# Kernel tuning notes

Hardware: AMD Instinct MI355X
Metric: run time of the kernel (lower is better)

Reference implementation:

```python
import jax, jax.numpy as jnp
import numpy as np

B, S, D, H = 2, 2048, 1024, 16
DK = D // H

def setup_inputs() -> dict:
    key = jax.random.key(0)
    ks = jax.random.split(key, 9)
    s = 1.0 / np.sqrt(D)
    return {
        "query": jax.random.normal(ks[0], (B, S, D), dtype=jnp.float32),
        "Wq": jax.random.uniform(ks[1], (D, D), jnp.float32, -s, s),
        "bq": jax.random.uniform(ks[2], (D,), jnp.float32, -s, s),
        "Wk": jax.random.uniform(ks[3], (D, D), jnp.float32, -s, s),
        "bk": jax.random.uniform(ks[4], (D,), jnp.float32, -s, s),
        "Wv": jax.random.uniform(ks[5], (D, D), jnp.float32, -s, s),
        "bv": jax.random.uniform(ks[6], (D,), jnp.float32, -s, s),
        "Wo": jax.random.uniform(ks[7], (D, D), jnp.float32, -s, s),
        "bo": jax.random.uniform(ks[8], (D,), jnp.float32, -s, s),
    }

def reference(query, Wq, bq, Wk, bk, Wv, bv, Wo, bo):
    # q/k/v projections, reshape to [B,H,S,DK]
    def proj(x, W, b):
        return (x @ W + b).reshape(B, S, H, DK).transpose(0, 2, 1, 3)
    q = proj(query, Wq, bq)
    k = proj(query, Wk, bk)
    v = proj(query, Wv, bv)
    scores = jnp.einsum("bhqd,bhkd->bhqk", q, k) / jnp.sqrt(jnp.float32(DK))
    attn = jax.nn.softmax(scores, axis=-1)
    out = jnp.einsum("bhqk,bhkd->bhqd", attn, v)  # [B,H,S,DK]
    concat = out.transpose(0, 2, 1, 3).reshape(B, S, D)
    return concat @ Wo + bo
```

## Files before the change

kernel.cpp:

```cpp
#include <hip/hip_runtime.h>

#define S_LEN  2048
#define DMODEL 1024
#define NHEAD  16
#define DKDIM  64
#define NBATCH 2

typedef short bf16x8 __attribute__((ext_vector_type(8)));
typedef float f32x4  __attribute__((ext_vector_type(4)));

__device__ __forceinline__ unsigned short f2b(float f){
  unsigned int x = __float_as_uint(f);
  return (unsigned short)((x + 0x7FFFu + ((x >> 16) & 1u)) >> 16);
}
__device__ __forceinline__ unsigned short f2b_rhu(float f){
  return (unsigned short)((__float_as_uint(f) + 0x8000u) >> 16);
}
__device__ __forceinline__ bf16x8 ld8(const unsigned short* p){
  return *reinterpret_cast<const bf16x8*>(p);
}
__device__ __forceinline__ void gld16(const unsigned short* g, unsigned short* l){
  __builtin_amdgcn_global_load_lds(
      (const __attribute__((address_space(1))) unsigned int*)(uintptr_t)g,
      (__attribute__((address_space(3))) unsigned int*)(uintptr_t)l,
      16, 0, 0);
}

__global__ __launch_bounds__(256) void convert_x(
    const float* __restrict__ X, unsigned short* __restrict__ Xc)
{
  const size_t i0 = ((size_t)blockIdx.x * 256 + threadIdx.x) * 8;
  const float4 a = *reinterpret_cast<const float4*>(X + i0);
  const float4 b = *reinterpret_cast<const float4*>(X + i0 + 4);
  bf16x8 o;
  o[0]=(short)f2b(a.x); o[1]=(short)f2b(a.y); o[2]=(short)f2b(a.z); o[3]=(short)f2b(a.w);
  o[4]=(short)f2b(b.x); o[5]=(short)f2b(b.y); o[6]=(short)f2b(b.z); o[7]=(short)f2b(b.w);
  *reinterpret_cast<bf16x8*>(Xc + i0) = o;
}

__global__ __launch_bounds__(256) void transpose_w(
    const float* __restrict__ W0, const float* __restrict__ W1,
    const float* __restrict__ W2, const float* __restrict__ W3,
    unsigned short* __restrict__ Wt)
{
  __shared__ unsigned short tile[64][65];
  const float* src = (blockIdx.z==0)?W0:(blockIdx.z==1)?W1:(blockIdx.z==2)?W2:W3;
  unsigned short* dst = Wt + (size_t)blockIdx.z * DMODEL * DMODEL;
  const int r0 = blockIdx.x * 64, c0 = blockIdx.y * 64;
  #pragma unroll
  for(int t=0;t<16;t++){
    int idx = threadIdx.x + t*256;
    int r = idx >> 6, c = idx & 63;
    tile[r][c] = f2b(src[(size_t)(r0+r)*DMODEL + (c0+c)]);
  }
  __syncthreads();
  #pragma unroll
  for(int t=0;t<16;t++){
    int idx = threadIdx.x + t*256;
    int r = idx >> 6, c = idx & 63;
    dst[(size_t)(c0+r)*DMODEL + (r0+c)] = tile[c][r];
  }
}

__global__ __launch_bounds__(256) void gemm_qkv(
    const unsigned short* __restrict__ Xc,
    const unsigned short* __restrict__ WtBase,
    const float* __restrict__ bq,
    const float* __restrict__ bk,
    const float* __restrict__ bv,
    unsigned short* __restrict__ q_ws,
    unsigned short* __restrict__ k_ws,
    unsigned short* __restrict__ vT_ws)
{
  __shared__ __align__(16) unsigned short sA[128][32];
  __shared__ __align__(16) unsigned short sB[128][32];
  const int z = blockIdx.z;
  const unsigned short* Wt   = WtBase + (size_t)z * DMODEL * DMODEL;
  const float* bias = (z==0) ? bq : ((z==1) ? bk : bv);
  const int m0 = blockIdx.x * 128, n0 = blockIdx.y * 128;
  const int tid = threadIdx.x;
  const int w = tid >> 6, lane = tid & 63, quad = lane >> 4, lm = lane & 15;
  const int wm = (w & 1) * 64, wn = (w >> 1) * 64;
  const int srow = lane >> 2, scol = (lane & 3) * 8;

  f32x4 acc[4][4];
  #pragma unroll
  for(int i=0;i<4;i++)
    #pragma unroll
    for(int j=0;j<4;j++){ f32x4 z4 = {0.f,0.f,0.f,0.f}; acc[i][j] = z4; }

  for(int k0=0;k0<DMODEL;k0+=32){
    #pragma unroll
    for(int j=0;j<2;j++){
      gld16(Xc + (size_t)(m0 + w*32 + j*16 + srow)*DMODEL + k0 + scol, &sA[w*32 + j*16][0]);
      gld16(Wt + (size_t)(n0 + w*32 + j*16 + srow)*DMODEL + k0 + scol, &sB[w*32 + j*16][0]);
    }
    __syncthreads();
    bf16x8 a[4], b[4];
    #pragma unroll
    for(int i=0;i<4;i++) a[i] = ld8(&sA[wm + i*16 + lm][quad*8]);
    #pragma unroll
    for(int j=0;j<4;j++) b[j] = ld8(&sB[wn + j*16 + lm][quad*8]);
    #pragma unroll
    for(int i=0;i<4;i++)
      #pragma unroll
      for(int j=0;j<4;j++)
        acc[i][j] = __builtin_amdgcn_mfma_f32_16x16x32_bf16(a[i], b[j], acc[i][j], 0, 0, 0);
    __syncthreads();
  }

  #pragma unroll
  for(int j=0;j<4;j++){
    const int n  = n0 + wn + j*16 + lm;
    const float bb = bias[n];
    const int h_ = n >> 6, d_ = n & 63;
    #pragma unroll
    for(int i=0;i<4;i++){
      #pragma unroll
      for(int r=0;r<4;r++){
        const int m  = m0 + wm + i*16 + quad*4 + r;
        const int b_ = m >> 11, s_ = m & 2047;
        const unsigned short o = f2b(acc[i][j][r] + bb);
        if(z == 0)      q_ws [((size_t)(b_*NHEAD + h_)*S_LEN + s_)*DKDIM + d_] = o;
        else if(z == 1) k_ws [((size_t)(b_*NHEAD + h_)*S_LEN + s_)*DKDIM + d_] = o;
        else            vT_ws[((size_t)(b_*NHEAD + h_)*DKDIM + d_)*S_LEN + s_] = o;
      }
    }
  }
}

__global__ __launch_bounds__(256) void flash_attn(
    const unsigned short* __restrict__ q_ws,
    const unsigned short* __restrict__ k_ws,
    const unsigned short* __restrict__ vT_ws,
    unsigned short* __restrict__ attn_c)
{
  __shared__ __align__(16) unsigned short kt[2][64][72];
  __shared__ __align__(16) unsigned short vt[2][64][72];
  __shared__ __align__(16) unsigned short p_lds[4][32][72];
  const int bh = blockIdx.y;
  const int b_ = bh >> 4, h_ = bh & 15;
  const int tid = threadIdx.x;
  const int w = tid >> 6, lane = tid & 63, quad = lane >> 4, lm = lane & 15;
  const int r0 = blockIdx.x * 128 + w * 32;

  const unsigned short* qp = q_ws  + ((size_t)bh * S_LEN + r0) * DKDIM;
  const unsigned short* kp = k_ws  + (size_t)bh * S_LEN * DKDIM;
  const unsigned short* vp = vT_ws + (size_t)bh * DKDIM * S_LEN;

  bf16x8 qf[2][2];
  #pragma unroll
  for(int g=0;g<2;g++)
    #pragma unroll
    for(int c=0;c<2;c++)
      qf[g][c] = ld8(qp + (size_t)(g*16 + lm)*DKDIM + c*32 + quad*8);

  f32x4 o_acc[2][4];
  #pragma unroll
  for(int g=0;g<2;g++)
    #pragma unroll
    for(int d=0;d<4;d++){ f32x4 z4 = {0.f,0.f,0.f,0.f}; o_acc[g][d] = z4; }
  float rsum[2][4] = {{0.f,0.f,0.f,0.f},{0.f,0.f,0.f,0.f}};

  const int srow = lane >> 3;
  const int scol = (lane & 7) * 8;

  bf16x8 kreg[2], vreg[2];
  #pragma unroll
  for(int p=0;p<2;p++){
    kreg[p] = ld8(kp + (size_t)(w*16 + p*8 + srow)*DKDIM + scol);
    vreg[p] = ld8(vp + (size_t)(w*16 + p*8 + srow)*S_LEN + scol);
  }
  #pragma unroll
  for(int p=0;p<2;p++){
    *reinterpret_cast<bf16x8*>(&kt[0][w*16 + p*8 + srow][scol]) = kreg[p];
    *reinterpret_cast<bf16x8*>(&vt[0][w*16 + p*8 + srow][scol]) = vreg[p];
  }
  __syncthreads();

  for(int t=0;t<32;t++){
    const int buf = t & 1;
    if(t < 31){
      const int jn = (t+1)*64;
      #pragma unroll
      for(int p=0;p<2;p++){
        kreg[p] = ld8(kp + (size_t)(jn + w*16 + p*8 + srow)*DKDIM + scol);
        vreg[p] = ld8(vp + (size_t)(w*16 + p*8 + srow)*S_LEN + jn + scol);
      }
    }
    #pragma unroll
    for(int s=0;s<4;s++){
      bf16x8 k0 = ld8(&kt[buf][s*16 + lm][quad*8]);
      bf16x8 k1 = ld8(&kt[buf][s*16 + lm][32 + quad*8]);
      #pragma unroll
      for(int g=0;g<2;g++){
        f32x4 z4 = {0.f,0.f,0.f,0.f};
        f32x4 sc = __builtin_amdgcn_mfma_f32_16x16x32_bf16(qf[g][0], k0, z4, 0,0,0);
        sc       = __builtin_amdgcn_mfma_f32_16x16x32_bf16(qf[g][1], k1, sc, 0,0,0);
        #pragma unroll
        for(int r=0;r<4;r++){
          float e = __expf(sc[r]*0.125f);
          rsum[g][r] += e;
          p_lds[w][g*16 + quad*4 + r][s*16 + lm] = f2b_rhu(e);
        }
      }
    }
    #pragma unroll
    for(int ch=0;ch<2;ch++){
      bf16x8 pf0 = ld8(&p_lds[w][lm     ][ch*32 + quad*8]);
      bf16x8 pf1 = ld8(&p_lds[w][16 + lm][ch*32 + quad*8]);
      #pragma unroll
      for(int d=0;d<4;d++){
        bf16x8 vf = ld8(&vt[buf][d*16 + lm][ch*32 + quad*8]);
        o_acc[0][d] = __builtin_amdgcn_mfma_f32_16x16x32_bf16(pf0, vf, o_acc[0][d], 0,0,0);
        o_acc[1][d] = __builtin_amdgcn_mfma_f32_16x16x32_bf16(pf1, vf, o_acc[1][d], 0,0,0);
      }
    }
    if(t < 31){
      const int nb = 1 - buf;
      #pragma unroll
      for(int p=0;p<2;p++){
        *reinterpret_cast<bf16x8*>(&kt[nb][w*16 + p*8 + srow][scol]) = kreg[p];
        *reinterpret_cast<bf16x8*>(&vt[nb][w*16 + p*8 + srow][scol]) = vreg[p];
      }
    }
    __syncthreads();
  }

  float rinv[2][4];
  #pragma unroll
  for(int g=0;g<2;g++)
    #pragma unroll
    for(int r=0;r<4;r++){
      float s = rsum[g][r];
      s += __shfl_xor(s,1);
      s += __shfl_xor(s,2);
      s += __shfl_xor(s,4);
      s += __shfl_xor(s,8);
      rinv[g][r] = __frcp_rn(s);
    }

  #pragma unroll
  for(int g=0;g<2;g++)
    #pragma unroll
    for(int d=0;d<4;d++)
      #pragma unroll
      for(int r=0;r<4;r++){
        const int row = r0 + g*16 + quad*4 + r;
        const int col = h_*DKDIM + d*16 + lm;
        attn_c[((size_t)(b_*S_LEN + row))*DMODEL + col] = f2b(o_acc[g][d][r] * rinv[g][r]);
      }
}

__global__ __launch_bounds__(256) void gemm_out(
    const unsigned short* __restrict__ A,
    const unsigned short* __restrict__ Wt,
    const float* __restrict__ bias,
    float* __restrict__ out)
{
  __shared__ __align__(16) unsigned short sA[128][32];
  __shared__ __align__(16) unsigned short sB[128][32];
  const int m0 = blockIdx.x * 128, n0 = blockIdx.y * 128;
  const int tid = threadIdx.x;
  const int w = tid >> 6, lane = tid & 63, quad = lane >> 4, lm = lane & 15;
  const int wm = (w & 1) * 64, wn = (w >> 1) * 64;
  const int srow = lane >> 2, scol = (lane & 3) * 8;

  f32x4 acc[4][4];
  #pragma unroll
  for(int i=0;i<4;i++)
    #pragma unroll
    for(int j=0;j<4;j++){ f32x4 z4 = {0.f,0.f,0.f,0.f}; acc[i][j] = z4; }

  for(int k0=0;k0<DMODEL;k0+=32){
    #pragma unroll
    for(int j=0;j<2;j++){
      gld16(A  + (size_t)(m0 + w*32 + j*16 + srow)*DMODEL + k0 + scol, &sA[w*32 + j*16][0]);
      gld16(Wt + (size_t)(n0 + w*32 + j*16 + srow)*DMODEL + k0 + scol, &sB[w*32 + j*16][0]);
    }
    __syncthreads();
    bf16x8 a[4], b[4];
    #pragma unroll
    for(int i=0;i<4;i++) a[i] = ld8(&sA[wm + i*16 + lm][quad*8]);
    #pragma unroll
    for(int j=0;j<4;j++) b[j] = ld8(&sB[wn + j*16 + lm][quad*8]);
    #pragma unroll
    for(int i=0;i<4;i++)
      #pragma unroll
      for(int j=0;j<4;j++)
        acc[i][j] = __builtin_amdgcn_mfma_f32_16x16x32_bf16(a[i], b[j], acc[i][j], 0, 0, 0);
    __syncthreads();
  }

  #pragma unroll
  for(int j=0;j<4;j++){
    const int n = n0 + wn + j*16 + lm;
    const float bb = bias[n];
    #pragma unroll
    for(int i=0;i<4;i++){
      #pragma unroll
      for(int r=0;r<4;r++){
        const int m = m0 + wm + i*16 + quad*4 + r;
        out[(size_t)m*DMODEL + n] = acc[i][j][r] + bb;
      }
    }
  }
}

extern "C" void kernel_launch(void* const* d_in, const int* in_sizes, int n_in,
                              void* d_out, int out_size, void* d_ws, size_t ws_size,
                              hipStream_t stream)
{
  const float* X  = (const float*)d_in[0];
  const float* Wq = (const float*)d_in[1];
  const float* bq = (const float*)d_in[2];
  const float* Wk = (const float*)d_in[3];
  const float* bk = (const float*)d_in[4];
  const float* Wv = (const float*)d_in[5];
  const float* bv = (const float*)d_in[6];
  const float* Wo = (const float*)d_in[7];
  const float* bo = (const float*)d_in[8];

  unsigned short* ws = (unsigned short*)d_ws;
  const size_t WMAT = (size_t)DMODEL * DMODEL;
  const size_t QKV  = (size_t)NBATCH * NHEAD * S_LEN * DKDIM;
  unsigned short* Wt     = ws;
  unsigned short* Xc     = ws + 4*WMAT;
  unsigned short* q_ws   = Xc + QKV;
  unsigned short* k_ws   = q_ws + QKV;
  unsigned short* vT_ws  = k_ws + QKV;
  unsigned short* attn_c = Xc;
  float* out = (float*)d_out;

  convert_x  <<<dim3(2048),     256, 0, stream>>>(X, Xc);
  transpose_w<<<dim3(16,16,4),  256, 0, stream>>>(Wq, Wk, Wv, Wo, Wt);
  gemm_qkv   <<<dim3(32,8,3),   256, 0, stream>>>(Xc, Wt, bq, bk, bv, q_ws, k_ws, vT_ws);
  flash_attn <<<dim3(16,32),    256, 0, stream>>>(q_ws, k_ws, vT_ws, attn_c);
  gemm_out   <<<dim3(32,8),     256, 0, stream>>>(attn_c, Wt + 3*WMAT, bo, out);
}
```

Baseline: 217.9 us.

## Transpose score MFMA, fold softmax scale into Q projection, swizzle packed P stores

Folds the 1/sqrt(dk) scale into the Q projection epilogue, so the attention loop exponentiates raw scores. It swaps the MFMA operands so each lane holds four consecutive keys of one query row. Those four bf16 probabilities are packed into one 8-byte LDS store into an XOR-swizzled P buffer, replacing four scalar 2-byte stores. Row sums now become per-lane scalars reduced with fewer shuffles at the end, at the cost of a different rounding path for Q.

```diff
diff --git a/kernel.cpp b/kernel.cpp
--- a/kernel.cpp
+++ b/kernel.cpp
@@ -12,9 +12,6 @@
 __device__ __forceinline__ unsigned short f2b(float f){
   unsigned int x = __float_as_uint(f);
   return (unsigned short)((x + 0x7FFFu + ((x >> 16) & 1u)) >> 16);
-}
-__device__ __forceinline__ unsigned short f2b_rhu(float f){
-  return (unsigned short)((__float_as_uint(f) + 0x8000u) >> 16);
 }
 __device__ __forceinline__ bf16x8 ld8(const unsigned short* p){
   return *reinterpret_cast<const bf16x8*>(p);
@@ -77,6 +74,7 @@
   const int z = blockIdx.z;
   const unsigned short* Wt   = WtBase + (size_t)z * DMODEL * DMODEL;
   const float* bias = (z==0) ? bq : ((z==1) ? bk : bv);
+  const float scl = (z==0) ? 0.125f : 1.0f;
   const int m0 = blockIdx.x * 128, n0 = blockIdx.y * 128;
   const int tid = threadIdx.x;
   const int w = tid >> 6, lane = tid & 63, quad = lane >> 4, lm = lane & 15;
@@ -112,7 +110,7 @@
   #pragma unroll
   for(int j=0;j<4;j++){
     const int n  = n0 + wn + j*16 + lm;
-    const float bb = bias[n];
+    const float bb = bias[n] * scl;
     const int h_ = n >> 6, d_ = n & 63;
     #pragma unroll
     for(int i=0;i<4;i++){
@@ -120,7 +118,7 @@
       for(int r=0;r<4;r++){
         const int m  = m0 + wm + i*16 + quad*4 + r;
         const int b_ = m >> 11, s_ = m & 2047;
-        const unsigned short o = f2b(acc[i][j][r] + bb);
+        const unsigned short o = f2b(fmaf(acc[i][j][r], scl, bb));
         if(z == 0)      q_ws [((size_t)(b_*NHEAD + h_)*S_LEN + s_)*DKDIM + d_] = o;
         else if(z == 1) k_ws [((size_t)(b_*NHEAD + h_)*S_LEN + s_)*DKDIM + d_] = o;
         else            vT_ws[((size_t)(b_*NHEAD + h_)*DKDIM + d_)*S_LEN + s_] = o;
@@ -137,12 +135,13 @@
 {
   __shared__ __align__(16) unsigned short kt[2][64][72];
   __shared__ __align__(16) unsigned short vt[2][64][72];
-  __shared__ __align__(16) unsigned short p_lds[4][32][72];
+  __shared__ __align__(16) unsigned short p_lds[4*32*64];
   const int bh = blockIdx.y;
   const int b_ = bh >> 4, h_ = bh & 15;
   const int tid = threadIdx.x;
   const int w = tid >> 6, lane = tid & 63, quad = lane >> 4, lm = lane & 15;
   const int r0 = blockIdx.x * 128 + w * 32;
+  const int swz = lm & 14;
 
   const unsigned short* qp = q_ws  + ((size_t)bh * S_LEN + r0) * DKDIM;
   const unsigned short* kp = k_ws  + (size_t)bh * S_LEN * DKDIM;
@@ -160,7 +159,7 @@
   for(int g=0;g<2;g++)
     #pragma unroll
     for(int d=0;d<4;d++){ f32x4 z4 = {0.f,0.f,0.f,0.f}; o_acc[g][d] = z4; }
-  float rsum[2][4] = {{0.f,0.f,0.f,0.f},{0.f,0.f,0.f,0.f}};
+  float rsum[2] = {0.f, 0.f};
 
   const int srow = lane >> 3;
   const int scol = (lane & 7) * 8;
@@ -195,20 +194,29 @@
       #pragma unroll
       for(int g=0;g<2;g++){
         f32x4 z4 = {0.f,0.f,0.f,0.f};
-        f32x4 sc = __builtin_amdgcn_mfma_f32_16x16x32_bf16(qf[g][0], k0, z4, 0,0,0);
-        sc       = __builtin_amdgcn_mfma_f32_16x16x32_bf16(qf[g][1], k1, sc, 0,0,0);
-        #pragma unroll
-        for(int r=0;r<4;r++){
-          float e = __expf(sc[r]*0.125f);
-          rsum[g][r] += e;
-          p_lds[w][g*16 + quad*4 + r][s*16 + lm] = f2b_rhu(e);
-        }
+        f32x4 sc = __builtin_amdgcn_mfma_f32_16x16x32_bf16(k0, qf[g][0], z4, 0,0,0);
+        sc       = __builtin_amdgcn_mfma_f32_16x16x32_bf16(k1, qf[g][1], sc, 0,0,0);
+        const float e0 = __expf(sc[0]);
+        const float e1 = __expf(sc[1]);
+        const float e2 = __expf(sc[2]);
+        const float e3 = __expf(sc[3]);
+        rsum[g] += (e0 + e1) + (e2 + e3);
+        const unsigned int u0 = __float_as_uint(e0) + 0x8000u;
+        const unsigned int u1 = __float_as_uint(e1) + 0x8000u;
+        const unsigned int u2 = __float_as_uint(e2) + 0x8000u;
+        const unsigned int u3 = __float_as_uint(e3) + 0x8000u;
+        uint2 pk;
+        pk.x = __builtin_amdgcn_perm(u1, u0, 0x07060302u);
+        pk.y = __builtin_amdgcn_perm(u3, u2, 0x07060302u);
+        *reinterpret_cast<uint2*>(
+          &p_lds[((w*32 + g*16 + lm) << 6) + (((s*4 + quad) ^ swz) << 2)]) = pk;
       }
     }
     #pragma unroll
     for(int ch=0;ch<2;ch++){
-      bf16x8 pf0 = ld8(&p_lds[w][lm     ][ch*32 + quad*8]);
-      bf16x8 pf1 = ld8(&p_lds[w][16 + lm][ch*32 + quad*8]);
+      const int sl = ((ch*8 + quad*2) ^ swz) << 2;
+      bf16x8 pf0 = ld8(&p_lds[((w*32      + lm) << 6) + sl]);
+      bf16x8 pf1 = ld8(&p_lds[((w*32 + 16 + lm) << 6) + sl]);
       #pragma unroll
       for(int d=0;d<4;d++){
         bf16x8 vf = ld8(&vt[buf][d*16 + lm][ch*32 + quad*8]);
@@ -229,16 +237,14 @@
 
   float rinv[2][4];
   #pragma unroll
-  for(int g=0;g<2;g++)
-    #pragma unroll
-    for(int r=0;r<4;r++){
-      float s = rsum[g][r];
-      s += __shfl_xor(s,1);
-      s += __shfl_xor(s,2);
-      s += __shfl_xor(s,4);
-      s += __shfl_xor(s,8);
-      rinv[g][r] = __frcp_rn(s);
-    }
+  for(int g=0;g<2;g++){
+    float s2 = rsum[g];
+    s2 += __shfl_xor(s2, 16);
+    s2 += __shfl_xor(s2, 32);
+    #pragma unroll
+    for(int r=0;r<4;r++)
+      rinv[g][r] = __frcp_rn(__shfl(s2, quad*4 + r));
+  }
 
   #pragma unroll
   for(int g=0;g<2;g++)
```

Result: faster. 207.9 us (-4.6%).
